# Kernel optimization log

Hardware: AMD Instinct MI355X
Metric: run time of the kernel (lower is better)

## Reference

```python
import jax, jax.numpy as jnp
import numpy as np

B, T, D = 4, 2048, 1024


def setup_inputs() -> dict:
    key = jax.random.key(0)
    ks = jax.random.split(key, 14)
    s = 0.02
    return {
        "x": jax.random.normal(ks[0], (B, T, D), dtype=jnp.float32),
        "time_decay": jax.random.normal(ks[1], (D,), dtype=jnp.float32) * 0.1,
        "tm_k": jax.random.uniform(ks[2], (D,), dtype=jnp.float32),
        "tm_v": jax.random.uniform(ks[3], (D,), dtype=jnp.float32),
        "tm_r": jax.random.uniform(ks[4], (D,), dtype=jnp.float32),
        "Wk": jax.random.normal(ks[5], (D, D), dtype=jnp.float32) * s,
        "Wv": jax.random.normal(ks[6], (D, D), dtype=jnp.float32) * s,
        "Wr": jax.random.normal(ks[7], (D, D), dtype=jnp.float32) * s,
        "Wo": jax.random.normal(ks[8], (D, D), dtype=jnp.float32) * s,
        "cm_k": jax.random.uniform(ks[9], (D,), dtype=jnp.float32),
        "cm_r": jax.random.uniform(ks[10], (D,), dtype=jnp.float32),
        "Wck": jax.random.normal(ks[11], (D, 4 * D), dtype=jnp.float32) * s,
        "Wcv": jax.random.normal(ks[12], (4 * D, D), dtype=jnp.float32) * s,
        "Wcr": jax.random.normal(ks[13], (D, D), dtype=jnp.float32) * s,
    }


def _shift(x):
    # token shift: prepend zero state (initial last_x), drop last token
    return jnp.concatenate([jnp.zeros_like(x[:, :1]), x[:, :-1]], axis=1)


def reference(x, time_decay, tm_k, tm_v, tm_r, Wk, Wv, Wr, Wo,
              cm_k, cm_r, Wck, Wcv, Wcr):
    # ---- time mixing (WKV recurrence) ----
    shifted = _shift(x)
    xk = x * tm_k + shifted * (1.0 - tm_k)
    xv = x * tm_v + shifted * (1.0 - tm_v)
    xr = x * tm_r + shifted * (1.0 - tm_r)
    k = xk @ Wk            # (B,T,D)
    v = xv @ Wv
    r = jax.nn.sigmoid(xr @ Wr)
    ew = jnp.exp(-jnp.exp(time_decay))  # exp(w), w = -exp(time_decay)

    def step(carry, kv):
        num, den = carry
        kt, vt = kv
        ek = jnp.exp(kt)
        num = ew * num + ek * vt
        den = ew * den + ek
        return (num, den), num / (den + 1e-6)

    init = (jnp.zeros((B, D), x.dtype), jnp.zeros((B, D), x.dtype))
    _, wkv_t = jax.lax.scan(step, init, (jnp.swapaxes(k, 0, 1), jnp.swapaxes(v, 0, 1)))
    wkv = jnp.swapaxes(wkv_t, 0, 1)  # (B,T,D)
    x = x + (r * wkv) @ Wo

    # ---- channel mixing (gated FFN, squared ReLU) ----
    shifted2 = _shift(x)
    xk2 = x * cm_k + shifted2 * (1.0 - cm_k)
    xr2 = x * cm_r + shifted2 * (1.0 - cm_r)
    kh = jnp.square(jax.nn.relu(xk2 @ Wck))  # (B,T,4D)
    v2 = kh @ Wcv
    r2 = jax.nn.sigmoid(xr2 @ Wcr)
    return x + r2 * v2
```

## Files before the change

kernel.cpp:

```cpp
#include <hip/hip_runtime.h>
#include <hip/hip_bf16.h>
#include <math.h>

#define BATCH 4
#define TLEN  2048
#define DIM   1024
#define NROWS (BATCH*TLEN)
#define HDIM  (4*DIM)

typedef __hip_bfloat16 bf16;
typedef __attribute__((ext_vector_type(8))) short   shortx8;
typedef __attribute__((ext_vector_type(4))) float   floatx4;

__device__ __forceinline__ unsigned short f2bf(float f) {
    bf16 h = __float2bfloat16(f);
    return __builtin_bit_cast(unsigned short, h);
}

__device__ __forceinline__ void async16(const void* g, void* l) {
    __builtin_amdgcn_global_load_lds((const __attribute__((address_space(1))) void*)g,
                                     (__attribute__((address_space(3))) void*)l, 16, 0, 0);
}

enum { EP_NONE=0, EP_SIGMOID=1, EP_ADD=2, EP_SQRELU=3, EP_FINAL=4 };

typedef const __attribute__((address_space(3))) char* lds3_t;


#define G_REGB   24576
#define G_ABYTES 8192
#define G_NSH    (5*12288)

__device__ __forceinline__ void gemm_core(
    const bf16* __restrict__ A, const bf16* __restrict__ Bt, const int K,
    const size_t m0, const size_t n0, short* lds, floatx4 (&acc)[4][4])
{
    const int tid = threadIdx.x;
    char* ldsc = (char*)lds;

    const int rA = tid >> 2;
    const int kA = ((tid & 3) ^ ((rA >> 1) & 3)) << 3;
    const bf16* pA  = A  + (size_t)(m0 + rA) * K + kA;
    const int s1  = 512 + tid;
    const int rB1 = s1 >> 2;
    const int kB1 = ((s1 & 3) ^ ((rB1 >> 1) & 3)) << 3;
    const bf16* pB0 = Bt + (size_t)(n0 + rA)  * K + kA;
    const bf16* pB1 = Bt + (size_t)(n0 + rB1) * K + kB1;
    char* dA  = ldsc + tid * 16;
    char* dB0 = ldsc + G_ABYTES + tid * 16;
    char* dB1 = ldsc + G_ABYTES + 8192 + tid * 16;

    const int lane = tid & 63;
    const int wave = tid >> 6;
    const int wm = (wave >> 2) * 64;
    const int wn = (wave & 3) * 64;
    const int lr = lane & 15, kq = lane >> 4;
    int offA[4], offB[4];
    #pragma unroll
    for (int i = 0; i < 4; ++i) {
        const int ra = wm + i*16 + lr;
        offA[i] = ra*64 + ((kq ^ ((ra>>1)&3)) << 4);
        const int rb = wn + i*16 + lr;
        offB[i] = G_ABYTES + rb*64 + ((kq ^ ((rb>>1)&3)) << 4);
    }

    const int P = K >> 5;

    auto stage = [&](int sl, int reg) {
        const int rB = reg * G_REGB;
        const int ko = sl << 5;
        async16(pA  + ko, dA  + rB);
        async16(pB0 + ko, dB0 + rB);
        async16(pB1 + ko, dB1 + rB);
    };
    auto ldfrag = [&](int reg, shortx8 (&af)[4], shortx8 (&bf_)[4]) {
        const char* rb = ldsc + (size_t)(reg * G_REGB);
        #pragma unroll
        for (int i = 0; i < 4; ++i) {
            lds3_t p = (lds3_t)(rb + offA[i]);
            asm volatile("ds_read_b128 %0, %1" : "=v"(af[i]) : "v"(p));
        }
        #pragma unroll
        for (int i = 0; i < 4; ++i) {
            lds3_t p = (lds3_t)(rb + offB[i]);
            asm volatile("ds_read_b128 %0, %1" : "=v"(bf_[i]) : "v"(p));
        }
    };
    auto domfma = [&](const shortx8 (&af)[4], const shortx8 (&bf_)[4]) {
        __builtin_amdgcn_s_setprio(1);
        #pragma unroll
        for (int mi = 0; mi < 4; ++mi)
            #pragma unroll
            for (int ni = 0; ni < 4; ++ni)
                acc[mi][ni] = __builtin_amdgcn_mfma_f32_16x16x32_bf16(
                                  af[mi], bf_[ni], acc[mi][ni], 0, 0, 0);
        __builtin_amdgcn_s_setprio(0);
    };

    stage(0,0); stage(1,1); stage(2,2); stage(3,3);
    asm volatile("s_waitcnt vmcnt(6)" ::: "memory");
    __builtin_amdgcn_s_barrier();
    __builtin_amdgcn_sched_barrier(0);

    shortx8 fa0[4], fb0[4], fa1[4], fb1[4];
    ldfrag(0, fa0, fb0);

    int cur = 0;
    for (int q = 0; q < P - 4; q += 2) {
        {
            const int sreg = (cur == 0) ? 4 : cur - 1;
            stage(q + 4, sreg);
            const int nxt = (cur == 4) ? 0 : cur + 1;
            ldfrag(nxt, fa1, fb1);
            asm volatile("s_waitcnt lgkmcnt(8)" ::: "memory");
            __builtin_amdgcn_sched_barrier(0);
            domfma(fa0, fb0);
            asm volatile("s_waitcnt vmcnt(6)" ::: "memory");
            __builtin_amdgcn_s_barrier();
            __builtin_amdgcn_sched_barrier(0);
            cur = nxt;
        }
        {
            const int sreg = (cur == 0) ? 4 : cur - 1;
            stage(q + 5, sreg);
            const int nxt = (cur == 4) ? 0 : cur + 1;
            ldfrag(nxt, fa0, fb0);
            asm volatile("s_waitcnt lgkmcnt(8)" ::: "memory");
            __builtin_amdgcn_sched_barrier(0);
            domfma(fa1, fb1);
            asm volatile("s_waitcnt vmcnt(6)" ::: "memory");
            __builtin_amdgcn_s_barrier();
            __builtin_amdgcn_sched_barrier(0);
            cur = nxt;
        }
    }

    {
        const int r1 = (cur == 4) ? 0 : cur + 1;
        ldfrag(r1, fa1, fb1);
        asm volatile("s_waitcnt lgkmcnt(8)" ::: "memory");
        __builtin_amdgcn_sched_barrier(0);
        domfma(fa0, fb0);
        asm volatile("s_waitcnt vmcnt(3)" ::: "memory");
        __builtin_amdgcn_s_barrier();
        __builtin_amdgcn_sched_barrier(0);
        const int r2 = (r1 == 4) ? 0 : r1 + 1;
        ldfrag(r2, fa0, fb0);
        asm volatile("s_waitcnt lgkmcnt(8)" ::: "memory");
        __builtin_amdgcn_sched_barrier(0);
        domfma(fa1, fb1);
        asm volatile("s_waitcnt vmcnt(0)" ::: "memory");
        __builtin_amdgcn_s_barrier();
        __builtin_amdgcn_sched_barrier(0);
        const int r3 = (r2 == 4) ? 0 : r2 + 1;
        ldfrag(r3, fa1, fb1);
        asm volatile("s_waitcnt lgkmcnt(8)" ::: "memory");
        __builtin_amdgcn_sched_barrier(0);
        domfma(fa0, fb0);
        asm volatile("s_waitcnt lgkmcnt(0)" ::: "memory");
        __builtin_amdgcn_sched_barrier(0);
        domfma(fa1, fb1);
    }
}

template<int MODE, typename OutT>
__device__ __forceinline__ void epilogue(
    floatx4 (&acc)[4][4], OutT* __restrict__ C,
    const float* __restrict__ addv, const bf16* __restrict__ mulv,
    const size_t m0, const size_t n0, const int N)
{
    const int tid = threadIdx.x;
    const int lane = tid & 63, wave = tid >> 6;
    const size_t r0 = m0 + (size_t)(wave >> 2) * 64 + ((lane >> 4) << 2);
    const size_t c0 = n0 + (size_t)(wave & 3) * 64 + (lane & 15);
    #pragma unroll
    for (int mi = 0; mi < 4; ++mi)
      #pragma unroll
      for (int ni = 0; ni < 4; ++ni)
        #pragma unroll
        for (int r = 0; r < 4; ++r) {
            const size_t off = (r0 + mi*16 + r) * N + c0 + ni*16;
            float v = acc[mi][ni][r];
            if (MODE == EP_SIGMOID)      v = 1.0f / (1.0f + __expf(-v));
            else if (MODE == EP_ADD)     v = addv[off] + v;
            else if (MODE == EP_SQRELU)  { float t = fmaxf(v, 0.0f); v = t * t; }
            else if (MODE == EP_FINAL)   v = addv[off] + __bfloat162float(mulv[off]) * v;
            if (sizeof(OutT) == 2) *(unsigned short*)(C + off) = f2bf(v);
            else                   *(float*)(C + off) = v;
        }
}

template<int MODE, typename OutT>
__global__ __launch_bounds__(512, 2)
void gemm256(const bf16* __restrict__ A, const bf16* __restrict__ Bt,
             OutT* __restrict__ C,
             const float* __restrict__ addv, const bf16* __restrict__ mulv,
             int N, int K)
{
    __shared__ __align__(16) short lds[G_NSH];
    const int nwg  = gridDim.x * gridDim.y;
    const int orig = blockIdx.y * gridDim.x + blockIdx.x;
    const int wg   = (orig & 7) * (nwg >> 3) + (orig >> 3);
    const int bx   = wg % gridDim.x;
    const int by   = wg / gridDim.x;
    const size_t m0 = (size_t)bx * 128;
    const size_t n0 = (size_t)by * 256;
    floatx4 acc[4][4] = {};
    gemm_core(A, Bt, K, m0, n0, lds, acc);
    epilogue<MODE, OutT>(acc, C, addv, mulv, m0, n0, N);
}

#define H_REGB   32768
#define H_ABYTES 16384
#define H_NSH    (4*16384)

#define DSR128(dst, p, OFF) \
    asm volatile("ds_read_b128 %0, %1 offset:" OFF : "=v"(dst) : "v"(p))

__device__ __forceinline__ void gemm_core_big(
    const bf16* __restrict__ A, const bf16* __restrict__ Bt, const int K,
    const size_t m0, const size_t n0, short* lds, floatx4 (&acc)[8][4])
{
    const int tid = threadIdx.x;
    char* ldsc = (char*)lds;

    const int rA0 = tid >> 2;
    const int rA1 = 128 + rA0;
    const int kg0 = ((tid & 3) ^ ((rA0 >> 1) & 3)) << 3;
    const int kg1 = ((tid & 3) ^ ((rA1 >> 1) & 3)) << 3;
    const bf16* pA0 = A  + (size_t)(m0 + rA0) * K + kg0;
    const bf16* pA1 = A  + (size_t)(m0 + rA1) * K + kg1;
    const bf16* pB0 = Bt + (size_t)(n0 + rA0) * K + kg0;
    const bf16* pB1 = Bt + (size_t)(n0 + rA1) * K + kg1;
    char* dA0 = ldsc + tid * 16;
    char* dA1 = ldsc + (512 + tid) * 16;
    char* dB0 = ldsc + H_ABYTES + tid * 16;
    char* dB1 = ldsc + H_ABYTES + (512 + tid) * 16;

    const int lane = tid & 63, wave = tid >> 6;
    const int wm = (wave >> 2) * 128;
    const int wn = (wave & 3) * 64;
    const int lr = lane & 15, kq = lane >> 4;
    const int ra0 = wm + lr;
    const int offA0 = ra0 * 64 + ((kq ^ ((ra0 >> 1) & 3)) << 4);
    const int rb0 = wn + lr;
    const int offB0 = H_ABYTES + rb0 * 64 + ((kq ^ ((rb0 >> 1) & 3)) << 4);

    const int P = K >> 5;

    auto stage = [&](int sl, int reg) {
        const int rb = reg * H_REGB;
        const int ko = sl << 5;
        async16(pA0 + ko, dA0 + rb);
        async16(pA1 + ko, dA1 + rb);
        async16(pB0 + ko, dB0 + rb);
        async16(pB1 + ko, dB1 + rb);
    };
    auto ldfrag = [&](int reg, shortx8 (&af)[8], shortx8 (&bf_)[4]) {
        lds3_t pa = (lds3_t)(ldsc + reg * H_REGB + offA0);
        lds3_t pb = (lds3_t)(ldsc + reg * H_REGB + offB0);
        DSR128(af[0], pa, "0");    DSR128(af[1], pa, "1024");
        DSR128(af[2], pa, "2048"); DSR128(af[3], pa, "3072");
        DSR128(af[4], pa, "4096"); DSR128(af[5], pa, "5120");
        DSR128(af[6], pa, "6144"); DSR128(af[7], pa, "7168");
        DSR128(bf_[0], pb, "0");    DSR128(bf_[1], pb, "1024");
        DSR128(bf_[2], pb, "2048"); DSR128(bf_[3], pb, "3072");
    };
    auto domfma = [&](const shortx8 (&af)[8], const shortx8 (&bf_)[4]) {
        __builtin_amdgcn_s_setprio(1);
        #pragma unroll
        for (int mi = 0; mi < 8; ++mi)
            #pragma unroll
            for (int ni = 0; ni < 4; ++ni)
                acc[mi][ni] = __builtin_amdgcn_mfma_f32_16x16x32_bf16(
                                  af[mi], bf_[ni], acc[mi][ni], 0, 0, 0);
        __builtin_amdgcn_s_setprio(0);
    };

    stage(0, 0); stage(1, 1); stage(2, 2);
    asm volatile("s_waitcnt vmcnt(4)" ::: "memory");
    __builtin_amdgcn_s_barrier();
    __builtin_amdgcn_sched_barrier(0);

    shortx8 fa0[8], fb0[4], fa1[8], fb1[4];
    ldfrag(0, fa0, fb0);

    int q = 0;
    for (; q + 1 < P - 3; q += 2) {
        stage(q + 3, (q + 3) & 3);
        ldfrag((q + 1) & 3, fa1, fb1);
        asm volatile("s_waitcnt lgkmcnt(12)" ::: "memory");
        __builtin_amdgcn_sched_barrier(0);
        domfma(fa0, fb0);
        asm volatile("s_waitcnt vmcnt(4)" ::: "memory");
        __builtin_amdgcn_s_barrier();
        __builtin_amdgcn_sched_barrier(0);
        stage(q + 4, (q + 4) & 3);
        ldfrag((q + 2) & 3, fa0, fb0);
        asm volatile("s_waitcnt lgkmcnt(12)" ::: "memory");
        __builtin_amdgcn_sched_barrier(0);
        domfma(fa1, fb1);
        asm volatile("s_waitcnt vmcnt(4)" ::: "memory");
        __builtin_amdgcn_s_barrier();
        __builtin_amdgcn_sched_barrier(0);
    }
    {
        stage(q + 3, (q + 3) & 3);
        ldfrag((q + 1) & 3, fa1, fb1);
        asm volatile("s_waitcnt lgkmcnt(12)" ::: "memory");
        __builtin_amdgcn_sched_barrier(0);
        domfma(fa0, fb0);
        asm volatile("s_waitcnt vmcnt(4)" ::: "memory");
        __builtin_amdgcn_s_barrier();
        __builtin_amdgcn_sched_barrier(0);
    }
    {
        ldfrag((q + 2) & 3, fa0, fb0);
        asm volatile("s_waitcnt lgkmcnt(12)" ::: "memory");
        __builtin_amdgcn_sched_barrier(0);
        domfma(fa1, fb1);
        asm volatile("s_waitcnt vmcnt(0)" ::: "memory");
        __builtin_amdgcn_s_barrier();
        __builtin_amdgcn_sched_barrier(0);
        ldfrag((q + 3) & 3, fa1, fb1);
        asm volatile("s_waitcnt lgkmcnt(12)" ::: "memory");
        __builtin_amdgcn_sched_barrier(0);
        domfma(fa0, fb0);
        asm volatile("s_waitcnt lgkmcnt(0)" ::: "memory");
        __builtin_amdgcn_sched_barrier(0);
        domfma(fa1, fb1);
    }
}

template<int MODE, typename OutT>
__device__ __forceinline__ void epilogueBig(
    floatx4 (&acc)[8][4], OutT* __restrict__ C,
    const float* __restrict__ addv, const bf16* __restrict__ mulv,
    const size_t m0, const size_t n0, const int N)
{
    const int tid = threadIdx.x;
    const int lane = tid & 63, wave = tid >> 6;
    const size_t r0 = m0 + (size_t)(wave >> 2) * 128 + ((lane >> 4) << 2);
    const size_t c0 = n0 + (size_t)(wave & 3) * 64 + (lane & 15);
    #pragma unroll
    for (int mi = 0; mi < 8; ++mi)
      #pragma unroll
      for (int ni = 0; ni < 4; ++ni)
        #pragma unroll
        for (int r = 0; r < 4; ++r) {
            const size_t off = (r0 + mi*16 + r) * N + c0 + ni*16;
            float v = acc[mi][ni][r];
            if (MODE == EP_SIGMOID)      v = 1.0f / (1.0f + __expf(-v));
            else if (MODE == EP_ADD)     v = addv[off] + v;
            else if (MODE == EP_SQRELU)  { float t = fmaxf(v, 0.0f); v = t * t; }
            else if (MODE == EP_FINAL)   v = addv[off] + __bfloat162float(mulv[off]) * v;
            if (sizeof(OutT) == 2) *(unsigned short*)(C + off) = f2bf(v);
            else                   *(float*)(C + off) = v;
        }
}

template<int MODE, typename OutT>
__global__ __launch_bounds__(512, 2)
void gemmBig(const bf16* __restrict__ A, const bf16* __restrict__ Bt,
             OutT* __restrict__ C,
             const float* __restrict__ addv, const bf16* __restrict__ mulv,
             int N, int K)
{
    __shared__ __align__(16) short lds[H_NSH];
    const int nwg  = gridDim.x * gridDim.y;
    const int orig = blockIdx.y * gridDim.x + blockIdx.x;
    const int wg   = (orig & 7) * (nwg >> 3) + (orig >> 3);
    const int bx   = wg % gridDim.x;
    const int by   = wg / gridDim.x;
    const size_t m0 = (size_t)bx * 256;
    const size_t n0 = (size_t)by * 256;
    floatx4 acc[8][4] = {};
    gemm_core_big(A, Bt, K, m0, n0, lds, acc);
    epilogueBig<MODE, OutT>(acc, C, addv, mulv, m0, n0, N);
}

struct GDesc { const bf16* A; const bf16* Bt; bf16* C; int mode; };
struct GArgs { GDesc d[3]; };

__global__ __launch_bounds__(512, 2)
void gemmBig_multi(GArgs args)
{
    __shared__ __align__(16) short lds[H_NSH];
    const int nwg  = gridDim.x * gridDim.y;
    const int orig = blockIdx.y * gridDim.x + blockIdx.x;
    const int wg   = (orig & 7) * (nwg >> 3) + (orig >> 3);
    const int bx   = wg % gridDim.x;
    const int byg  = wg / gridDim.x;
    const int di   = byg >> 2;
    const int by   = byg & 3;
    const GDesc d  = args.d[di];
    const size_t m0 = (size_t)bx * 256;
    const size_t n0 = (size_t)by * 256;
    floatx4 acc[8][4] = {};
    gemm_core_big(d.A, d.Bt, DIM, m0, n0, lds, acc);

    const int tid = threadIdx.x;
    const int lane = tid & 63, wave = tid >> 6;
    const size_t r0 = m0 + (size_t)(wave >> 2) * 128 + ((lane >> 4) << 2);
    const size_t c0 = n0 + (size_t)(wave & 3) * 64 + (lane & 15);
    const bool sig = (d.mode == EP_SIGMOID);
    #pragma unroll
    for (int mi = 0; mi < 8; ++mi)
      #pragma unroll
      for (int ni = 0; ni < 4; ++ni)
        #pragma unroll
        for (int r = 0; r < 4; ++r) {
            const size_t off = (r0 + mi*16 + r) * DIM + c0 + ni*16;
            float v = acc[mi][ni][r];
            if (sig) v = 1.0f / (1.0f + __expf(-v));
            *(unsigned short*)(d.C + off) = f2bf(v);
        }
}

struct TDesc { const float* in; bf16* out; int K; int N; int tiles; int tx; };
struct PrepArgs {
    TDesc t[7];
    int ttotal;
    const float4 *x, *mk, *mv, *mr;
    ushort4 *ok, *ov, *orr;
};

__global__ __launch_bounds__(256)
void prep_kernel(PrepArgs a)
{
    int blk = blockIdx.x;
    if (blk < a.ttotal) {
        int t = blk, di = 0;
        while (t >= a.t[di].tiles) { t -= a.t[di].tiles; ++di; }
        const float* in  = a.t[di].in;
        bf16*        out = a.t[di].out;
        const int K = a.t[di].K, N = a.t[di].N, tx = a.t[di].tx;
        const int bx = t % tx, by = t / tx;
        __shared__ float tile[32][33];
        const int kt = by * 32, nt = bx * 32;
        #pragma unroll
        for (int i = threadIdx.y; i < 32; i += 8)
            tile[i][threadIdx.x] = in[(size_t)(kt + i) * N + nt + threadIdx.x];
        __syncthreads();
        #pragma unroll
        for (int i = threadIdx.y; i < 32; i += 8)
            out[(size_t)(nt + i) * K + kt + threadIdx.x] =
                __float2bfloat16(tile[threadIdx.x][i]);
    } else {
        const int D4 = DIM / 4;
        int tid = threadIdx.y * 32 + threadIdx.x;
        int e   = (blk - a.ttotal) * 256 + tid;
        int d4  = e & (D4 - 1);
        int t   = (e >> 8) & (TLEN - 1);
        float4 xc = a.x[e];
        float4 sh = make_float4(0.f, 0.f, 0.f, 0.f);
        if (t > 0) sh = a.x[e - D4];
        float4 mk = a.mk[d4], mv = a.mv[d4], mr = a.mr[d4];
        ushort4 u;
        u.x=f2bf(xc.x*mk.x+sh.x*(1.f-mk.x)); u.y=f2bf(xc.y*mk.y+sh.y*(1.f-mk.y));
        u.z=f2bf(xc.z*mk.z+sh.z*(1.f-mk.z)); u.w=f2bf(xc.w*mk.w+sh.w*(1.f-mk.w));
        a.ok[e]=u;
        u.x=f2bf(xc.x*mv.x+sh.x*(1.f-mv.x)); u.y=f2bf(xc.y*mv.y+sh.y*(1.f-mv.y));
        u.z=f2bf(xc.z*mv.z+sh.z*(1.f-mv.z)); u.w=f2bf(xc.w*mv.w+sh.w*(1.f-mv.w));
        a.ov[e]=u;
        u.x=f2bf(xc.x*mr.x+sh.x*(1.f-mr.x)); u.y=f2bf(xc.y*mr.y+sh.y*(1.f-mr.y));
        u.z=f2bf(xc.z*mr.z+sh.z*(1.f-mr.z)); u.w=f2bf(xc.w*mr.w+sh.w*(1.f-mr.w));
        a.orr[e]=u;
    }
}

__global__ __launch_bounds__(256)
void mix2_kernel(const float4* __restrict__ x,
                 const float4* __restrict__ mk, const float4* __restrict__ mr,
                 ushort4* __restrict__ ok, ushort4* __restrict__ orr)
{
    const int D4 = DIM / 4;
    int e   = blockIdx.x * 256 + threadIdx.x;
    int d4  = e & (D4 - 1);
    int t   = (e >> 8) & (TLEN - 1);
    float4 xc = x[e];
    float4 sh = make_float4(0.f, 0.f, 0.f, 0.f);
    if (t > 0) sh = x[e - D4];
    float4 a = mk[d4], c = mr[d4];
    ushort4 u;
    u.x=f2bf(xc.x*a.x+sh.x*(1.f-a.x)); u.y=f2bf(xc.y*a.y+sh.y*(1.f-a.y));
    u.z=f2bf(xc.z*a.z+sh.z*(1.f-a.z)); u.w=f2bf(xc.w*a.w+sh.w*(1.f-a.w));
    ok[e]=u;
    u.x=f2bf(xc.x*c.x+sh.x*(1.f-c.x)); u.y=f2bf(xc.y*c.y+sh.y*(1.f-c.y));
    u.z=f2bf(xc.z*c.z+sh.z*(1.f-c.z)); u.w=f2bf(xc.w*c.w+sh.w*(1.f-c.w));
    orr[e]=u;
}

#define WKV_CHUNK 64
#define WKV_WARM  64
__global__ __launch_bounds__(256)
void wkv_kernel(const bf16* __restrict__ K, const bf16* __restrict__ V,
                const bf16* __restrict__ R, const float* __restrict__ td,
                bf16* __restrict__ out)
{
    int d     = blockIdx.x * 256 + threadIdx.x;
    int chunk = blockIdx.y;
    int b     = blockIdx.z;
    int start = chunk * WKV_CHUNK;
    int t0    = start - WKV_WARM; if (t0 < 0) t0 = 0;

    float ew = __expf(-__expf(td[d]));
    float num = 0.f, den = 0.f;
    size_t base = ((size_t)b * TLEN) * DIM + d;

    for (int t = t0; t < start; ++t) {
        size_t idx = base + (size_t)t * DIM;
        float ek = __expf(__bfloat162float(K[idx]));
        num = ew * num + ek * __bfloat162float(V[idx]);
        den = ew * den + ek;
    }
    for (int t = start; t < start + WKV_CHUNK; ++t) {
        size_t idx = base + (size_t)t * DIM;
        float ek = __expf(__bfloat162float(K[idx]));
        num = ew * num + ek * __bfloat162float(V[idx]);
        den = ew * den + ek;
        out[idx] = __float2bfloat16(__bfloat162float(R[idx]) * (num / (den + 1e-6f)));
    }
}

extern "C" void kernel_launch(void* const* d_in, const int* in_sizes, int n_in,
                              void* d_out, int out_size, void* d_ws, size_t ws_size,
                              hipStream_t stream)
{
    const float* x   = (const float*)d_in[0];
    const float* td  = (const float*)d_in[1];
    const float* tmk = (const float*)d_in[2];
    const float* tmv = (const float*)d_in[3];
    const float* tmr = (const float*)d_in[4];
    const float* Wk  = (const float*)d_in[5];
    const float* Wv  = (const float*)d_in[6];
    const float* Wr  = (const float*)d_in[7];
    const float* Wo  = (const float*)d_in[8];
    const float* cmk = (const float*)d_in[9];
    const float* cmr = (const float*)d_in[10];
    const float* Wck = (const float*)d_in[11];
    const float* Wcv = (const float*)d_in[12];
    const float* Wcr = (const float*)d_in[13];
    float* out = (float*)d_out;

    char* ws = (char*)d_ws;
    const size_t MB = 1024 * 1024;
    bf16*  Wk_t  = (bf16*)(ws +   0*MB);
    bf16*  Wv_t  = (bf16*)(ws +   2*MB);
    bf16*  Wr_t  = (bf16*)(ws +   4*MB);
    bf16*  Wo_t  = (bf16*)(ws +   6*MB);
    bf16*  Wcr_t = (bf16*)(ws +   8*MB);
    bf16*  Wck_t = (bf16*)(ws +  10*MB);
    bf16*  Wcv_t = (bf16*)(ws +  18*MB);
    float* f0    = (float*)(ws + 26*MB);
    bf16*  bA    = (bf16*)(ws +  58*MB);
    bf16*  bB    = (bf16*)(ws +  74*MB);
    bf16*  bC    = (bf16*)(ws +  90*MB);
    bf16*  bD    = (bf16*)(ws + 106*MB);
    bf16*  bE    = (bf16*)(ws + 122*MB);
    bf16*  bF    = (bf16*)(ws + 138*MB);
    bf16*  kh    = bA;

    const dim3 blk(256);
    const dim3 gblk(512);

    {
        PrepArgs pa;
        const float* src[7] = {Wk, Wv, Wr, Wo, Wcr, Wck, Wcv};
        bf16*        dst[7] = {Wk_t, Wv_t, Wr_t, Wo_t, Wcr_t, Wck_t, Wcv_t};
        int          kk[7]  = {DIM, DIM, DIM, DIM, DIM, DIM, HDIM};
        int          nn[7]  = {DIM, DIM, DIM, DIM, DIM, HDIM, DIM};
        int total = 0;
        for (int i = 0; i < 7; ++i) {
            int tx = nn[i] / 32, ty = kk[i] / 32;
            pa.t[i] = {src[i], dst[i], kk[i], nn[i], tx * ty, tx};
            total += tx * ty;
        }
        pa.ttotal = total;
        pa.x  = (const float4*)x;
        pa.mk = (const float4*)tmk; pa.mv = (const float4*)tmv; pa.mr = (const float4*)tmr;
        pa.ok = (ushort4*)bA; pa.ov = (ushort4*)bB; pa.orr = (ushort4*)bC;
        const int mixBlocks = NROWS * DIM / 4 / 256;
        prep_kernel<<<dim3(total + mixBlocks), dim3(32, 8), 0, stream>>>(pa);
    }

    {
        GArgs ga;
        ga.d[0] = {bA, Wk_t, bD, EP_NONE};
        ga.d[1] = {bB, Wv_t, bE, EP_NONE};
        ga.d[2] = {bC, Wr_t, bF, EP_SIGMOID};
        gemmBig_multi<<<dim3(NROWS/256, 12), gblk, 0, stream>>>(ga);
    }

    dim3 wkvGrid(DIM / 256, TLEN / WKV_CHUNK, BATCH);
    wkv_kernel<<<wkvGrid, blk, 0, stream>>>(bD, bE, bF, td, bF);

    gemm256<EP_ADD, float><<<dim3(NROWS/128, DIM/256), gblk, 0, stream>>>(
        bF, Wo_t, f0, x, nullptr, DIM, DIM);

    mix2_kernel<<<dim3(NROWS * DIM / 4 / 256), blk, 0, stream>>>(
        (const float4*)f0, (const float4*)cmk, (const float4*)cmr,
        (ushort4*)bE, (ushort4*)bA);

    gemm256<EP_SIGMOID, bf16><<<dim3(NROWS/128, DIM/256), gblk, 0, stream>>>(
        bA, Wcr_t, bF, nullptr, nullptr, DIM, DIM);

    gemmBig<EP_SQRELU, bf16><<<dim3(NROWS/256, HDIM/256), gblk, 0, stream>>>(
        bE, Wck_t, kh, nullptr, nullptr, HDIM, DIM);

    gemm256<EP_FINAL, float><<<dim3(NROWS/128, DIM/256), gblk, 0, stream>>>(
        kh, Wcv_t, out, f0, bF, DIM, HDIM);
}
```

Before: 485.5 us.

## Use 128x256 tiles for fused KVR GEMM and simplify big-GEMM fragment pipeline

```diff
diff --git a/kernel.cpp b/kernel.cpp
--- a/kernel.cpp
+++ b/kernel.cpp
@@ -208,6 +208,44 @@
     floatx4 acc[4][4] = {};
     gemm_core(A, Bt, K, m0, n0, lds, acc);
     epilogue<MODE, OutT>(acc, C, addv, mulv, m0, n0, N);
+}
+
+struct GDesc { const bf16* A; const bf16* Bt; bf16* C; int mode; };
+struct GArgs { GDesc d[3]; };
+
+__global__ __launch_bounds__(512, 2)
+void gemm256_multi(GArgs args)
+{
+    __shared__ __align__(16) short lds[G_NSH];
+    const int nwg  = gridDim.x * gridDim.y;
+    const int orig = blockIdx.y * gridDim.x + blockIdx.x;
+    const int wg   = (orig & 7) * (nwg >> 3) + (orig >> 3);
+    const int bx   = wg % gridDim.x;
+    const int byg  = wg / gridDim.x;
+    const int di   = byg >> 2;
+    const int by   = byg & 3;
+    const GDesc d  = args.d[di];
+    const size_t m0 = (size_t)bx * 128;
+    const size_t n0 = (size_t)by * 256;
+    floatx4 acc[4][4] = {};
+    gemm_core(d.A, d.Bt, DIM, m0, n0, lds, acc);
+
+    const int tid = threadIdx.x;
+    const int lane = tid & 63, wave = tid >> 6;
+    const size_t r0 = m0 + (size_t)(wave >> 2) * 64 + ((lane >> 4) << 2);
+    const size_t c0 = n0 + (size_t)(wave & 3) * 64 + (lane & 15);
+    const bool sig = (d.mode == EP_SIGMOID);
+    #pragma unroll
+    for (int mi = 0; mi < 4; ++mi)
+      #pragma unroll
+      for (int ni = 0; ni < 4; ++ni)
+        #pragma unroll
+        for (int r = 0; r < 4; ++r) {
+            const size_t off = (r0 + mi*16 + r) * DIM + c0 + ni*16;
+            float v = acc[mi][ni][r];
+            if (sig) v = 1.0f / (1.0f + __expf(-v));
+            *(unsigned short*)(d.C + off) = f2bf(v);
+        }
 }
 
 #define H_REGB   32768
@@ -278,58 +316,40 @@
     };
 
     stage(0, 0); stage(1, 1); stage(2, 2);
+    asm volatile("s_waitcnt vmcnt(8)" ::: "memory");
+    __builtin_amdgcn_s_barrier();
+    __builtin_amdgcn_sched_barrier(0);
+
+    shortx8 af[8], bf_[4];
+
+    for (int q = 0; q < P - 3; ++q) {
+        stage(q + 3, (q + 3) & 3);
+        ldfrag(q & 3, af, bf_);
+        asm volatile("s_waitcnt lgkmcnt(0)" ::: "memory");
+        __builtin_amdgcn_sched_barrier(0);
+        domfma(af, bf_);
+        asm volatile("s_waitcnt vmcnt(8)" ::: "memory");
+        __builtin_amdgcn_s_barrier();
+        __builtin_amdgcn_sched_barrier(0);
+    }
+    ldfrag((P - 3) & 3, af, bf_);
+    asm volatile("s_waitcnt lgkmcnt(0)" ::: "memory");
+    __builtin_amdgcn_sched_barrier(0);
+    domfma(af, bf_);
     asm volatile("s_waitcnt vmcnt(4)" ::: "memory");
     __builtin_amdgcn_s_barrier();
     __builtin_amdgcn_sched_barrier(0);
-
-    shortx8 fa0[8], fb0[4], fa1[8], fb1[4];
-    ldfrag(0, fa0, fb0);
-
-    int q = 0;
-    for (; q + 1 < P - 3; q += 2) {
-        stage(q + 3, (q + 3) & 3);
-        ldfrag((q + 1) & 3, fa1, fb1);
-        asm volatile("s_waitcnt lgkmcnt(12)" ::: "memory");
-        __builtin_amdgcn_sched_barrier(0);
-        domfma(fa0, fb0);
-        asm volatile("s_waitcnt vmcnt(4)" ::: "memory");
-        __builtin_amdgcn_s_barrier();
-        __builtin_amdgcn_sched_barrier(0);
-        stage(q + 4, (q + 4) & 3);
-        ldfrag((q + 2) & 3, fa0, fb0);
-        asm volatile("s_waitcnt lgkmcnt(12)" ::: "memory");
-        __builtin_amdgcn_sched_barrier(0);
-        domfma(fa1, fb1);
-        asm volatile("s_waitcnt vmcnt(4)" ::: "memory");
-        __builtin_amdgcn_s_barrier();
-        __builtin_amdgcn_sched_barrier(0);
-    }
-    {
-        stage(q + 3, (q + 3) & 3);
-        ldfrag((q + 1) & 3, fa1, fb1);
-        asm volatile("s_waitcnt lgkmcnt(12)" ::: "memory");
-        __builtin_amdgcn_sched_barrier(0);
-        domfma(fa0, fb0);
-        asm volatile("s_waitcnt vmcnt(4)" ::: "memory");
-        __builtin_amdgcn_s_barrier();
-        __builtin_amdgcn_sched_barrier(0);
-    }
-    {
-        ldfrag((q + 2) & 3, fa0, fb0);
-        asm volatile("s_waitcnt lgkmcnt(12)" ::: "memory");
-        __builtin_amdgcn_sched_barrier(0);
-        domfma(fa1, fb1);
-        asm volatile("s_waitcnt vmcnt(0)" ::: "memory");
-        __builtin_amdgcn_s_barrier();
-        __builtin_amdgcn_sched_barrier(0);
-        ldfrag((q + 3) & 3, fa1, fb1);
-        asm volatile("s_waitcnt lgkmcnt(12)" ::: "memory");
-        __builtin_amdgcn_sched_barrier(0);
-        domfma(fa0, fb0);
-        asm volatile("s_waitcnt lgkmcnt(0)" ::: "memory");
-        __builtin_amdgcn_sched_barrier(0);
-        domfma(fa1, fb1);
-    }
+    ldfrag((P - 2) & 3, af, bf_);
+    asm volatile("s_waitcnt lgkmcnt(0)" ::: "memory");
+    __builtin_amdgcn_sched_barrier(0);
+    domfma(af, bf_);
+    asm volatile("s_waitcnt vmcnt(0)" ::: "memory");
+    __builtin_amdgcn_s_barrier();
+    __builtin_amdgcn_sched_barrier(0);
+    ldfrag((P - 1) & 3, af, bf_);
+    asm volatile("s_waitcnt lgkmcnt(0)" ::: "memory");
+    __builtin_amdgcn_sched_barrier(0);
+    domfma(af, bf_);
 }
 
 template<int MODE, typename OutT>
@@ -377,44 +397,6 @@
     floatx4 acc[8][4] = {};
     gemm_core_big(A, Bt, K, m0, n0, lds, acc);
     epilogueBig<MODE, OutT>(acc, C, addv, mulv, m0, n0, N);
-}
-
-struct GDesc { const bf16* A; const bf16* Bt; bf16* C; int mode; };
-struct GArgs { GDesc d[3]; };
-
-__global__ __launch_bounds__(512, 2)
-void gemmBig_multi(GArgs args)
-{
-    __shared__ __align__(16) short lds[H_NSH];
-    const int nwg  = gridDim.x * gridDim.y;
-    const int orig = blockIdx.y * gridDim.x + blockIdx.x;
-    const int wg   = (orig & 7) * (nwg >> 3) + (orig >> 3);
-    const int bx   = wg % gridDim.x;
-    const int byg  = wg / gridDim.x;
-    const int di   = byg >> 2;
-    const int by   = byg & 3;
-    const GDesc d  = args.d[di];
-    const size_t m0 = (size_t)bx * 256;
-    const size_t n0 = (size_t)by * 256;
-    floatx4 acc[8][4] = {};
-    gemm_core_big(d.A, d.Bt, DIM, m0, n0, lds, acc);
-
-    const int tid = threadIdx.x;
-    const int lane = tid & 63, wave = tid >> 6;
-    const size_t r0 = m0 + (size_t)(wave >> 2) * 128 + ((lane >> 4) << 2);
-    const size_t c0 = n0 + (size_t)(wave & 3) * 64 + (lane & 15);
-    const bool sig = (d.mode == EP_SIGMOID);
-    #pragma unroll
-    for (int mi = 0; mi < 8; ++mi)
-      #pragma unroll
-      for (int ni = 0; ni < 4; ++ni)
-        #pragma unroll
-        for (int r = 0; r < 4; ++r) {
-            const size_t off = (r0 + mi*16 + r) * DIM + c0 + ni*16;
-            float v = acc[mi][ni][r];
-            if (sig) v = 1.0f / (1.0f + __expf(-v));
-            *(unsigned short*)(d.C + off) = f2bf(v);
-        }
 }
 
 struct TDesc { const float* in; bf16* out; int K; int N; int tiles; int tx; };
@@ -589,7 +571,7 @@
         ga.d[0] = {bA, Wk_t, bD, EP_NONE};
         ga.d[1] = {bB, Wv_t, bE, EP_NONE};
         ga.d[2] = {bC, Wr_t, bF, EP_SIGMOID};
-        gemmBig_multi<<<dim3(NROWS/256, 12), gblk, 0, stream>>>(ga);
+        gemm256_multi<<<dim3(NROWS/128, 12), gblk, 0, stream>>>(ga);
     }
 
     dim3 wkvGrid(DIM / 256, TLEN / WKV_CHUNK, BATCH);
```

Measured after the change: 477.8 us. Within noise of the previous version (-1.6%).
